# Performance work log

Hardware: AMD Instinct MI355X
Metric: run time of the kernel (lower is better)

Reference implementation:

```python
import jax, jax.numpy as jnp
import numpy as np

# ive(v, z) = exp(-|z|) * I_v(z), the exponentially scaled modified Bessel
# function of the first kind (matches scipy.special.ive for z > 0).
# Computed via the power series in log space for numerical stability:
#   I_v(z) = sum_k (z/2)^(v+2k) / (k! * Gamma(v+k+1))
# 256 terms is ample for v=63, z <= 200 (series peak at k ~ 70, rapid decay).

V = 63.0          # Bessel order: vMF latent dim 128 -> v = 128/2 - 1
K_TERMS = 256     # number of series terms
Z_MIN, Z_MAX = 0.1, 200.0


def setup_inputs() -> dict:
    key = jax.random.key(0)
    # positive concentrations kappa, per input_specs fill=rand scaled to [0.1, 200)
    z = jax.random.uniform(key, (1048576,), dtype=jnp.float32,
                           minval=Z_MIN, maxval=Z_MAX)
    return {"z": z}


def _log_ive(z):
    # z: [N] positive. Returns log(ive(V, z)) = log I_V(z) - z, shape [N].
    k = jnp.arange(K_TERMS, dtype=jnp.float32)                 # [K]
    log_half_z = jnp.log(0.5 * z)[..., None]                   # [N, 1]
    # log term_k = (v + 2k) log(z/2) - lgamma(k+1) - lgamma(v+k+1)
    log_terms = ((V + 2.0 * k) * log_half_z
                 - jax.lax.lgamma(k + 1.0)
                 - jax.lax.lgamma(V + k + 1.0))                # [N, K]
    return jax.scipy.special.logsumexp(log_terms, axis=-1) - z  # [N]


def reference(z):
    # Ive(v).forward(z) == scipy.special.ive(v, z) elementwise
    return jnp.exp(_log_ive(z))
```

## Files before the change

kernel.cpp:

```cpp
#include <hip/hip_runtime.h>


constexpr int BLOCK = 256;
constexpr int EPT   = 4;
constexpr int WIDTH = 28;
constexpr int TBL   = 128;

__global__ __launch_bounds__(BLOCK) void ive63_kernel(const float* __restrict__ zin,
                                                      float* __restrict__ out,
                                                      int n) {
    __shared__ float c_lds[TBL];
    __shared__ float rc_lds[TBL];
    if (threadIdx.x < TBL) {
        const float kf = (float)threadIdx.x;
        c_lds[threadIdx.x]  = lgammaf(kf + 1.0f) + lgammaf(kf + 64.0f);
        rc_lds[threadIdx.x] = 1.0f / ((kf + 1.0f) * (kf + 64.0f));
    }
    __syncthreads();

    const int base = (blockIdx.x * BLOCK + threadIdx.x) * EPT;
    if (base >= n) return;

    float zz[EPT];
    if (base + EPT <= n) {
        const float4 v = *reinterpret_cast<const float4*>(zin + base);
        zz[0] = v.x; zz[1] = v.y; zz[2] = v.z; zz[3] = v.w;
    } else {
        #pragma unroll
        for (int e = 0; e < EPT; ++e) zz[e] = (base + e < n) ? zin[base + e] : 1.0f;
    }

    float rr[EPT];
    #pragma unroll
    for (int e = 0; e < EPT; ++e) {
        const float z = zz[e];
        const float L    = __logf(0.5f * z);
        const float q    = 0.25f * z * z;
        const float qinv = 1.0f / q;

        int kc = (int)((sqrtf(fmaf(z, z, 3969.0f)) - 65.0f) * 0.5f);
        kc = kc < 0 ? 0 : (kc > 95 ? 95 : kc);

        const float logt = fmaf((float)(63 + 2 * kc), L, -c_lds[kc]);

        float u1 = 1.0f, u2 = 1.0f, S1 = 0.0f, S2 = 0.0f;
        float kd = (float)kc;
        const float* rcp = &rc_lds[kc];
        #pragma unroll
        for (int j = 0; j < WIDTH; ++j) {
            u1 *= q * rcp[j];
            S1 += u1;
            u2 *= (kd * (kd + 63.0f)) * qinv;
            S2 += u2;
            kd -= 1.0f;
        }
        const float S = 1.0f + S1 + S2;

        rr[e] = __expf(logt + __logf(S) - z);
    }

    if (base + EPT <= n) {
        *reinterpret_cast<float4*>(out + base) = make_float4(rr[0], rr[1], rr[2], rr[3]);
    } else {
        #pragma unroll
        for (int e = 0; e < EPT; ++e) if (base + e < n) out[base + e] = rr[e];
    }
}

extern "C" void kernel_launch(void* const* d_in, const int* in_sizes, int n_in,
                              void* d_out, int out_size, void* d_ws, size_t ws_size,
                              hipStream_t stream) {
    const float* z = (const float*)d_in[0];
    float* o = (float*)d_out;
    const int n = in_sizes[0];
    const int grid = (n + BLOCK * EPT - 1) / (BLOCK * EPT);
    hipLaunchKernelGGL(ive63_kernel, dim3(grid), dim3(BLOCK), 0, stream, z, o, n);
}
```

Before: 61.82 us.

## Replace truncated power series with uniform asymptotic expansion for I_63

Replaces the LDS-tabulated, centred 28-term power series with Debye's uniform asymptotic expansion for large order, using two correction terms. This removes the shared-memory table setup, the barrier, and the long per-element multiply-add chain, leaving a handful of transcendental and polynomial operations per element. The risk is accuracy: the expansion is truncated, so relative error at small z or mid-range z could exceed the tolerance. The kernel is memory-light, so cutting arithmetic should shorten it substantially.

```diff
diff --git a/kernel.cpp b/kernel.cpp
--- a/kernel.cpp
+++ b/kernel.cpp
@@ -3,21 +3,10 @@
 
 constexpr int BLOCK = 256;
 constexpr int EPT   = 4;
-constexpr int WIDTH = 28;
-constexpr int TBL   = 128;
 
 __global__ __launch_bounds__(BLOCK) void ive63_kernel(const float* __restrict__ zin,
                                                       float* __restrict__ out,
                                                       int n) {
-    __shared__ float c_lds[TBL];
-    __shared__ float rc_lds[TBL];
-    if (threadIdx.x < TBL) {
-        const float kf = (float)threadIdx.x;
-        c_lds[threadIdx.x]  = lgammaf(kf + 1.0f) + lgammaf(kf + 64.0f);
-        rc_lds[threadIdx.x] = 1.0f / ((kf + 1.0f) * (kf + 64.0f));
-    }
-    __syncthreads();
-
     const int base = (blockIdx.x * BLOCK + threadIdx.x) * EPT;
     if (base >= n) return;
 
@@ -33,30 +22,25 @@
     float rr[EPT];
     #pragma unroll
     for (int e = 0; e < EPT; ++e) {
-        const float z = zz[e];
-        const float L    = __logf(0.5f * z);
-        const float q    = 0.25f * z * z;
-        const float qinv = 1.0f / q;
+        const float z  = zz[e];
+        const float x  = z * (1.0f / 63.0f);
+        const float x2 = x * x;
+        const float s2 = 1.0f + x2;
+        const float t  = __frsqrt_rn(s2);
+        const float s  = s2 * t;
 
-        int kc = (int)((sqrtf(fmaf(z, z, 3969.0f)) - 65.0f) * 0.5f);
-        kc = kc < 0 ? 0 : (kc > 95 ? 95 : kc);
+        const float a    = s + __logf(x) - __logf(1.0f + s);
+        const float expo = fmaf(63.0f, a, -z);
 
-        const float logt = fmaf((float)(63 + 2 * kc), L, -c_lds[kc]);
+        const float pref = 0.05026201f * __fsqrt_rn(t);
 
-        float u1 = 1.0f, u2 = 1.0f, S1 = 0.0f, S2 = 0.0f;
-        float kd = (float)kc;
-        const float* rcp = &rc_lds[kc];
-        #pragma unroll
-        for (int j = 0; j < WIDTH; ++j) {
-            u1 *= q * rcp[j];
-            S1 += u1;
-            u2 *= (kd * (kd + 63.0f)) * qinv;
-            S2 += u2;
-            kd -= 1.0f;
-        }
-        const float S = 1.0f + S1 + S2;
+        const float t2 = t * t;
+        const float p1 = t * fmaf(-5.0f, t2, 3.0f) * (1.0f / 1512.0f);
+        const float q2 = fmaf(fmaf(385.0f, t2, -462.0f), t2, 81.0f);
+        const float p2 = t2 * q2 * (1.0f / 4572288.0f);
+        const float S  = 1.0f + p1 + p2;
 
-        rr[e] = __expf(logt + __logf(S) - z);
+        rr[e] = __expf(expo) * pref * S;
     }
 
     if (base + EPT <= n) {
```

New measurement: 55.47 us. -10.3%, faster.
